# Optimization experiments

Measured on AMD Instinct MI355X. Metric: run time of the kernel, lower is better.

## Reference

```python
import jax, jax.numpy as jnp
import numpy as np
import math

B, L, DM, H, DK, DV, T, PW = 2, 512, 256, 4, 64, 64, 8, 8


def setup_inputs() -> dict:
    key = jax.random.key(0)
    ks = jax.random.split(key, 16)
    q = jax.random.normal(ks[0], (B, L, DM), jnp.float32)
    k = jax.random.normal(ks[1], (B, L, DM), jnp.float32)
    v = jax.random.normal(ks[2], (B, L, DM), jnp.float32)
    # sorted timestamps in [0, 100]
    t_in = jnp.sort(jax.random.uniform(ks[3], (B, L), jnp.float32) * 100.0, axis=-1)
    c = jax.random.randint(ks[4], (B, L), 0, T).astype(jnp.int32)  # no padding tokens
    mask = jnp.broadcast_to(jnp.triu(jnp.ones((L, L), bool), 1)[None], (B, L, L))  # causal
    s_in = 1.0 / math.sqrt(DM)
    Wq = jax.random.normal(ks[5], (DM, H * DK), jnp.float32) * s_in
    Wk = jax.random.normal(ks[6], (DM, H * DK), jnp.float32) * s_in
    Wv = jax.random.normal(ks[7], (DM, H * DV), jnp.float32) * s_in
    Wo = jax.random.normal(ks[8], (H * DV, DM), jnp.float32) / math.sqrt(H * DV)
    ln_g = jnp.ones((DM,), jnp.float32)
    ln_b = jnp.zeros((DM,), jnp.float32)
    # per-(type, head) phi MLP: Linear(1->PW), GELU, Linear(PW->PW), GELU, Linear(PW->1)
    W0 = jax.random.normal(ks[9], (T, H, PW, 1), jnp.float32) * 0.1
    b0 = jax.random.normal(ks[10], (T, H, PW), jnp.float32) * 0.1
    W1 = jax.random.normal(ks[11], (T, H, PW, PW), jnp.float32) * 0.3
    b1 = jax.random.normal(ks[12], (T, H, PW), jnp.float32) * 0.1
    Wf = jax.random.normal(ks[13], (T, H, 1, PW), jnp.float32) * 0.3
    bf = jax.random.normal(ks[14], (T, H, 1), jnp.float32) * 0.1
    return dict(q=q, k=k, v=v, t_in=t_in, c=c, mask=mask, ln_g=ln_g, ln_b=ln_b,
                Wq=Wq, Wk=Wk, Wv=Wv, Wo=Wo, W0=W0, b0=b0, W1=W1, b1=b1, Wf=Wf, bf=bf)


def _gelu(x):
    return jax.nn.gelu(x, approximate=False)


def _forward(q, k, v, t_in, c, mask, ln_g, ln_b, Wq, Wk, Wv, Wo, W0, b0, W1, b1, Wf, bf):
    Bb, Ll, dm = q.shape
    num_types, Hh, pw, _ = W0.shape
    dk = Wq.shape[1] // Hh
    dv = Wv.shape[1] // Hh
    scale = math.sqrt(dk)
    residual = q
    # pre-LayerNorm on q only (normalize_before=True)
    mu = jnp.mean(q, -1, keepdims=True)
    var = jnp.mean((q - mu) ** 2, -1, keepdims=True)
    qn = (q - mu) / jnp.sqrt(var + 1e-6) * ln_g + ln_b
    qh = (qn @ Wq).reshape(Bb, Ll, Hh, dk).transpose(0, 2, 1, 3)  # (B,H,L,dk)
    kh = (k @ Wk).reshape(Bb, Ll, Hh, dk).transpose(0, 2, 1, 3)
    vh = (v @ Wv).reshape(Bb, Ll, Hh, dv).transpose(0, 2, 1, 3)
    delta = t_in[:, :, None] - t_in[:, None, :]  # (B,Li,Lj)
    valid = c < num_types
    vmask = valid[:, :, None] & valid[:, None, :]  # (B,Li,Lj)
    cs = jnp.clip(c, 0, num_types - 1)
    # gather per-token phi params -> leading dims (B,L,H,...)
    W0g = W0[cs][..., 0]          # (B,L,H,pw)
    b0g = b0[cs]                  # (B,L,H,pw)
    W1g = W1[cs]                  # (B,L,H,pw,pw)  [out,in]
    b1g = b1[cs]                  # (B,L,H,pw)
    Wfg = Wf[cs][:, :, :, 0, :]   # (B,L,H,pw)
    bfg = bf[cs][..., 0]          # (B,L,H)
    # phiQ[b,h,i,j] = phi_{c_i,h}(delta_ij)
    hq = _gelu(delta[:, :, None, :, None] * W0g[:, :, :, None, :] + b0g[:, :, :, None, :])  # (B,Li,H,Lj,pw)
    hq = _gelu(jnp.einsum('bihjw,bihuw->bihju', hq, W1g) + b1g[:, :, :, None, :])
    phiQ = jnp.einsum('bihjw,bihw->bihj', hq, Wfg) + bfg[:, :, :, None]  # (B,Li,H,Lj)
    phiQ = jnp.where(vmask[:, :, None, :], phiQ, 0.0).transpose(0, 2, 1, 3)  # (B,H,Li,Lj)
    # phiK[b,h,i,j] = phi_{c_j,h}(delta_ij)
    hk = _gelu(delta[:, :, :, None, None] * W0g[:, None, :, :, :] + b0g[:, None, :, :, :])  # (B,Li,Lj,H,pw)
    hk = _gelu(jnp.einsum('bijhw,bjhuw->bijhu', hk, W1g) + b1g[:, None, :, :, :])
    phiK = jnp.einsum('bijhw,bjhw->bijh', hk, Wfg) + bfg[:, None, :, :]  # (B,Li,Lj,H)
    phiK = jnp.where(vmask[:, :, :, None], phiK, 0.0).transpose(0, 3, 1, 2)  # (B,H,Li,Lj)
    # scores[b,h,i,j] = (q_i . k_j) * phiQ * phiK / scale  (equivalent to q_mod*k_mod sum)
    scores = jnp.einsum('bhid,bhjd->bhij', qh, kh) * phiQ * phiK / scale
    scores = jnp.where(mask[:, None, :, :], -jnp.inf, scores)
    attn = jax.nn.softmax(scores, axis=-1)
    # out_heads[b,h,i,d] = sum_j attn * phiK * v_j  (equivalent to einsum with v_mod)
    out_heads = jnp.einsum('bhij,bhjd->bhid', attn * phiK, vh)
    out = out_heads.transpose(0, 2, 1, 3).reshape(Bb, Ll, Hh * dv) @ Wo
    return out + residual


def reference(q, k, v, t_in, c, mask, ln_g, ln_b, Wq, Wk, Wv, Wo, W0, b0, W1, b1, Wf, bf):
    return _forward(q, k, v, t_in, c, mask, ln_g, ln_b, Wq, Wk, Wv, Wo, W0, b0, W1, b1, Wf, bf)
```

## Files before the change

### kernel.cpp

```cpp
#include <hip/hip_runtime.h>
#include <math.h>

#define B_  2
#define L_  512
#define DM_ 256
#define H_  4
#define DK_ 64
#define DV_ 64
#define T_  8
#define PW_ 8
#define NTAB 4096

typedef unsigned int uint;

__device__ __forceinline__ unsigned short f2b(float x) {
    uint u = __float_as_uint(x);
    u += 0x7fffu + ((u >> 16) & 1u);
    return (unsigned short)(u >> 16);
}
__device__ __forceinline__ float bl(uint u)  { return __uint_as_float(u << 16); }
__device__ __forceinline__ float bh_(uint u) { return __uint_as_float(u & 0xffff0000u); }

__device__ __forceinline__ float gelu_fast(float x) {
    const float z  = x * 0.70710678118654752440f;
    const float az = fabsf(z);
    const float t  = __builtin_amdgcn_rcpf(fmaf(0.3275911f, az, 1.0f));
    float p = fmaf(t, 1.061405429f, -1.453152027f);
    p = fmaf(t, p, 1.421413741f);
    p = fmaf(t, p, -0.284496736f);
    p = fmaf(t, p, 0.254829592f);
    p *= t;
    const float e  = __expf(-az * az);
    float er = fmaf(-p, e, 1.0f);
    er = copysignf(er, z);
    return 0.5f * x * (1.0f + er);
}

__device__ __forceinline__ float phi_eval_u(
        const float w0r[8], const float b0r[8], const float4* __restrict__ W14,
        const float b1r[8], const float wfr[8], float bfv, float delta) {
    float h1[PW_];
#pragma unroll
    for (int w = 0; w < PW_; ++w)
        h1[w] = gelu_fast(fmaf(delta, w0r[w], b0r[w]));
    float out = bfv;
#pragma unroll
    for (int u = 0; u < PW_; ++u) {
        const float4 c0 = W14[u * 2];
        const float4 c1 = W14[u * 2 + 1];
        float a = b1r[u];
        a = fmaf(c0.x, h1[0], a); a = fmaf(c0.y, h1[1], a);
        a = fmaf(c0.z, h1[2], a); a = fmaf(c0.w, h1[3], a);
        a = fmaf(c1.x, h1[4], a); a = fmaf(c1.y, h1[5], a);
        a = fmaf(c1.z, h1[6], a); a = fmaf(c1.w, h1[7], a);
        out = fmaf(wfr[u], gelu_fast(a), out);
    }
    return out;
}

__device__ __forceinline__ float tab_lerp(const float* __restrict__ tab, float delta) {
    float x = delta * ((float)(NTAB - 1) / 100.0f);
    x = fminf(fmaxf(x, 0.0f), (float)(NTAB - 1) - 0.001f);
    const int i0 = (int)x;
    const float f = x - (float)i0;
    const float a = tab[i0];
    const float b = tab[i0 + 1];
    return fmaf(b - a, f, a);
}

__global__ __launch_bounds__(256) void prep_kernel(
        const float* __restrict__ q, const float* __restrict__ k,
        const float* __restrict__ v, const float* __restrict__ ln_g,
        const float* __restrict__ ln_b, const float* __restrict__ Wq,
        const float* __restrict__ Wk, const float* __restrict__ Wv,
        const float* __restrict__ W0, const float* __restrict__ b0,
        const float* __restrict__ W1, const float* __restrict__ b1,
        const float* __restrict__ Wf, const float* __restrict__ bfp,
        float* __restrict__ qh, uint* __restrict__ khT,
        uint* __restrict__ vh8, float* __restrict__ tabs) {
    __shared__ __align__(16) float smem[8 * DM_];
    const int tid = threadIdx.x, lane = tid & 63, wv = tid >> 6;
    const int bx = blockIdx.x;

    if (bx < 512) {
        const int th = bx >> 4;
        const int p = (bx & 15) * 256 + tid;
        if (tid < 64) smem[tid] = W1[th * 64 + tid];
        float w0r[8], b0r[8], b1r[8], wfr[8];
#pragma unroll
        for (int w = 0; w < 8; ++w) {
            w0r[w] = W0[th * 8 + w]; b0r[w] = b0[th * 8 + w];
            b1r[w] = b1[th * 8 + w]; wfr[w] = Wf[th * 8 + w];
        }
        const float bfv = bfp[th];
        __syncthreads();
        const float delta = (float)p * (100.0f / (float)(NTAB - 1));
        tabs[th * NTAB + p] = phi_eval_u(w0r, b0r,
                                         reinterpret_cast<const float4*>(smem),
                                         b1r, wfr, bfv, delta);
    } else if (bx < 1024) {
        const bool isQ = (bx < 768);
        const int bid = isQ ? (bx - 512) : (bx - 768);
        float (*xr)[DM_] = reinterpret_cast<float (*)[DM_]>(smem);
        const int row0 = bid * 4;
        const int b = row0 >> 9;
        const int lrow0 = row0 & (L_ - 1);
        const float* src = isQ ? q : k;
        const float* W   = isQ ? Wq : Wk;
        for (int x = tid; x < 4 * DM_; x += 256)
            xr[x >> 8][x & 255] = src[(size_t)row0 * DM_ + x];
        __syncthreads();
        if (isQ) {
            const int r = wv;
            float x0 = xr[r][lane], x1 = xr[r][lane + 64];
            float x2 = xr[r][lane + 128], x3 = xr[r][lane + 192];
            float s = x0 + x1 + x2 + x3;
#pragma unroll
            for (int off = 32; off; off >>= 1) s += __shfl_xor(s, off);
            const float mean = s * (1.0f / 256.0f);
            x0 -= mean; x1 -= mean; x2 -= mean; x3 -= mean;
            float s2 = x0 * x0 + x1 * x1 + x2 * x2 + x3 * x3;
#pragma unroll
            for (int off = 32; off; off >>= 1) s2 += __shfl_xor(s2, off);
            const float rstd = rsqrtf(s2 * (1.0f / 256.0f) + 1e-6f);
            xr[r][lane]       = x0 * rstd * ln_g[lane]       + ln_b[lane];
            xr[r][lane + 64]  = x1 * rstd * ln_g[lane + 64]  + ln_b[lane + 64];
            xr[r][lane + 128] = x2 * rstd * ln_g[lane + 128] + ln_b[lane + 128];
            xr[r][lane + 192] = x3 * rstd * ln_g[lane + 192] + ln_b[lane + 192];
            __syncthreads();
        }
        float acc[4] = {0, 0, 0, 0};
#pragma unroll 8
        for (int kk = 0; kk < DM_; ++kk) {
            const float w = W[(size_t)kk * DM_ + tid];
#pragma unroll
            for (int r = 0; r < 4; ++r) acc[r] = fmaf(xr[r][kk], w, acc[r]);
        }
        if (isQ) {
#pragma unroll
            for (int r = 0; r < 4; ++r)
                qh[(size_t)(row0 + r) * DM_ + tid] = acc[r];
        } else {
            __syncthreads();
            unsigned short* sbuf = reinterpret_cast<unsigned short*>(smem);
#pragma unroll
            for (int r = 0; r < 4; ++r)
                sbuf[tid * 4 + r] = f2b(acc[r]);
            __syncthreads();
            if (tid < 128) {
                const int jl = tid & 3;
                const int g = tid >> 2;
                const int h2 = g >> 3, d8 = g & 7;
                unsigned short e[8];
#pragma unroll
                for (int ee = 0; ee < 8; ++ee)
                    e[ee] = sbuf[(h2 * 64 + d8 * 8 + ee) * 4 + jl];
                uint4 o;
                o.x = (uint)e[0] | ((uint)e[1] << 16);
                o.y = (uint)e[2] | ((uint)e[3] << 16);
                o.z = (uint)e[4] | ((uint)e[5] << 16);
                o.w = (uint)e[6] | ((uint)e[7] << 16);
                reinterpret_cast<uint4*>(khT)[
                    ((size_t)(b * H_ + h2) * 8 + d8) * L_ + lrow0 + jl] = o;
            }
        }
    } else {
        const int bid = bx - 1024;
        float (*xr)[DM_] = reinterpret_cast<float (*)[DM_]>(smem);
        const int row0 = bid * 8;
        const int b = row0 >> 9;
        const int lrow0 = row0 & (L_ - 1);
        for (int x = tid; x < 8 * DM_; x += 256)
            xr[x >> 8][x & 255] = v[(size_t)row0 * DM_ + x];
        __syncthreads();
        float acc[8] = {0, 0, 0, 0, 0, 0, 0, 0};
#pragma unroll 4
        for (int kk = 0; kk < DM_; ++kk) {
            const float w = Wv[(size_t)kk * DM_ + tid];
#pragma unroll
            for (int r = 0; r < 8; ++r) acc[r] = fmaf(xr[r][kk], w, acc[r]);
        }
        const int h = tid >> 6, d = tid & 63;
        const int bh = b * H_ + h;
        uint4 w4;
        w4.x = (uint)f2b(acc[0]) | ((uint)f2b(acc[1]) << 16);
        w4.y = (uint)f2b(acc[2]) | ((uint)f2b(acc[3]) << 16);
        w4.z = (uint)f2b(acc[4]) | ((uint)f2b(acc[5]) << 16);
        w4.w = (uint)f2b(acc[6]) | ((uint)f2b(acc[7]) << 16);
        reinterpret_cast<uint4*>(vh8)[((size_t)bh * 64 + (lrow0 >> 3)) * 64 + d] = w4;
    }
}

__global__ __launch_bounds__(64) void attn_kernel(
        const float* __restrict__ qh, const uint* __restrict__ khT,
        const uint* __restrict__ vh8, const float* __restrict__ t_in,
        const int* __restrict__ c, const float* __restrict__ tabs,
        float* __restrict__ oh) {
    __shared__ __align__(16) float qs[64];
    __shared__ __align__(16) float sw[L_];

    const int lane = threadIdx.x;
    const int unit = blockIdx.x;
    const int bh = unit & 7;
    const int b = bh >> 2, h = bh & 3;
    const int i = (L_ - 1) - (unit >> 3);
    const int row = b * L_ + i;

    qs[lane] = qh[(size_t)row * DM_ + h * DK_ + lane];
    const float ti = t_in[row];
    const int ciw = c[row];
    const bool vi = (ciw < T_);
    const float* tabQ = tabs + (size_t)(min(max(ciw, 0), T_ - 1) * H_ + h) * NTAB;
    __syncthreads();

    const float4* qs4 = reinterpret_cast<const float4*>(qs);
    const uint4* kT8 = reinterpret_cast<const uint4*>(khT) + (size_t)bh * 8 * L_;
    const float* tbase = t_in + b * L_;
    const int* cbase = c + b * L_;
    const int tmax = i >> 6;

    float s[8], pk[8];
    float m = -INFINITY;
#pragma unroll
    for (int t = 0; t < 8; ++t) {
        s[t] = -INFINITY; pk[t] = 0.0f;
        if (t <= tmax) {
            const int j = t * 64 + lane;
            const bool act = (j <= i);
            const float tj = tbase[j];
            const int cjw = cbase[j];
            const float* tabK = tabs + (size_t)(min(max(cjw, 0), T_ - 1) * H_ + h) * NTAB;
            const float delta = ti - tj;
            const float pq = vi ? tab_lerp(tabQ, delta) : 0.0f;
            const float pkv = (cjw < T_) ? tab_lerp(tabK, delta) : 0.0f;
            float dot = 0.0f;
#pragma unroll
            for (int d8 = 0; d8 < 8; ++d8) {
                const uint4 ku = kT8[(size_t)d8 * L_ + j];
                const float4 qa = qs4[2 * d8];
                const float4 qb = qs4[2 * d8 + 1];
                dot = fmaf(qa.x, bl(ku.x), fmaf(qa.y, bh_(ku.x),
                      fmaf(qa.z, bl(ku.y), fmaf(qa.w, bh_(ku.y), dot))));
                dot = fmaf(qb.x, bl(ku.z), fmaf(qb.y, bh_(ku.z),
                      fmaf(qb.z, bl(ku.w), fmaf(qb.w, bh_(ku.w), dot))));
            }
            if (act) { s[t] = dot * pq * pkv * 0.125f; pk[t] = pkv; }
            m = fmaxf(m, s[t]);
        }
    }
#pragma unroll
    for (int off = 32; off; off >>= 1) m = fmaxf(m, __shfl_xor(m, off));

    float l = 0.0f;
#pragma unroll
    for (int t = 0; t < 8; ++t) {
        if (t <= tmax) {
            const float e = __expf(s[t] - m);
            l += e;
            sw[t * 64 + lane] = e * pk[t];
        }
    }
#pragma unroll
    for (int off = 32; off; off >>= 1) l += __shfl_xor(l, off);
    __syncthreads();

    const uint4* vb = reinterpret_cast<const uint4*>(vh8) + (size_t)bh * 64 * 64 + lane;
    const int j8max = i >> 3;
    float a0 = 0.0f, a1 = 0.0f, a2 = 0.0f, a3 = 0.0f;
    int j8 = 0;
    for (; j8 + 1 <= j8max; j8 += 2) {
        const uint4 u0 = vb[(size_t)j8 * 64];
        const uint4 u1 = vb[(size_t)(j8 + 1) * 64];
        const float4 w0 = *reinterpret_cast<const float4*>(&sw[j8 * 8]);
        const float4 w1 = *reinterpret_cast<const float4*>(&sw[j8 * 8 + 4]);
        const float4 w2 = *reinterpret_cast<const float4*>(&sw[j8 * 8 + 8]);
        const float4 w3 = *reinterpret_cast<const float4*>(&sw[j8 * 8 + 12]);
        a0 = fmaf(w0.x, bl(u0.x), fmaf(w0.y, bh_(u0.x),
             fmaf(w0.z, bl(u0.y), fmaf(w0.w, bh_(u0.y), a0))));
        a1 = fmaf(w1.x, bl(u0.z), fmaf(w1.y, bh_(u0.z),
             fmaf(w1.z, bl(u0.w), fmaf(w1.w, bh_(u0.w), a1))));
        a2 = fmaf(w2.x, bl(u1.x), fmaf(w2.y, bh_(u1.x),
             fmaf(w2.z, bl(u1.y), fmaf(w2.w, bh_(u1.y), a2))));
        a3 = fmaf(w3.x, bl(u1.z), fmaf(w3.y, bh_(u1.z),
             fmaf(w3.z, bl(u1.w), fmaf(w3.w, bh_(u1.w), a3))));
    }
    for (; j8 <= j8max; ++j8) {
        const uint4 u = vb[(size_t)j8 * 64];
        const float4 w0 = *reinterpret_cast<const float4*>(&sw[j8 * 8]);
        const float4 w1 = *reinterpret_cast<const float4*>(&sw[j8 * 8 + 4]);
        a0 = fmaf(w0.x, bl(u.x), fmaf(w0.y, bh_(u.x),
             fmaf(w0.z, bl(u.y), fmaf(w0.w, bh_(u.y), a0))));
        a1 = fmaf(w1.x, bl(u.z), fmaf(w1.y, bh_(u.z),
             fmaf(w1.z, bl(u.w), fmaf(w1.w, bh_(u.w), a1))));
    }
    const float acc = (a0 + a1) + (a2 + a3);
    oh[(size_t)row * DM_ + h * DV_ + lane] = vi ? acc / l : 0.0f;
}

__global__ __launch_bounds__(256) void out4_kernel(const float* __restrict__ oh,
                                                   const float* __restrict__ Wo,
                                                   const float* __restrict__ q,
                                                   float* __restrict__ out) {
    __shared__ __align__(16) float xr[4][DM_];
    const int tid = threadIdx.x;
    const int row0 = blockIdx.x * 4;
    for (int x = tid; x < 4 * DM_; x += 256)
        xr[x >> 8][x & 255] = oh[(size_t)row0 * DM_ + x];
    __syncthreads();
    float acc[4] = {0, 0, 0, 0};
#pragma unroll 8
    for (int kk = 0; kk < DM_; ++kk) {
        const float w = Wo[(size_t)kk * DM_ + tid];
#pragma unroll
        for (int r = 0; r < 4; ++r) acc[r] = fmaf(xr[r][kk], w, acc[r]);
    }
#pragma unroll
    for (int r = 0; r < 4; ++r)
        out[(size_t)(row0 + r) * DM_ + tid] = acc[r] + q[(size_t)(row0 + r) * DM_ + tid];
}

extern "C" void kernel_launch(void* const* d_in, const int* in_sizes, int n_in,
                              void* d_out, int out_size, void* d_ws, size_t ws_size,
                              hipStream_t stream) {
    const float* q    = (const float*)d_in[0];
    const float* k    = (const float*)d_in[1];
    const float* v    = (const float*)d_in[2];
    const float* t_in = (const float*)d_in[3];
    const int*   c    = (const int*)d_in[4];
    const float* ln_g = (const float*)d_in[6];
    const float* ln_b = (const float*)d_in[7];
    const float* Wq   = (const float*)d_in[8];
    const float* Wk   = (const float*)d_in[9];
    const float* Wv   = (const float*)d_in[10];
    const float* Wo   = (const float*)d_in[11];
    const float* W0   = (const float*)d_in[12];
    const float* b0   = (const float*)d_in[13];
    const float* W1   = (const float*)d_in[14];
    const float* b1   = (const float*)d_in[15];
    const float* Wf   = (const float*)d_in[16];
    const float* bf   = (const float*)d_in[17];
    float* outp = (float*)d_out;

    const size_t SZ = (size_t)B_ * L_ * DM_;
    float* ws = (float*)d_ws;
    float* qh   = ws;
    uint*  khT  = (uint*)(ws + SZ);
    uint*  vh8  = (uint*)(ws + SZ + 131072);
    float* oh   = ws + SZ + 262144;
    float* tabs = ws + 2 * SZ + 262144;

    prep_kernel<<<dim3(1152), dim3(256), 0, stream>>>(
        q, k, v, ln_g, ln_b, Wq, Wk, Wv,
        W0, b0, W1, b1, Wf, bf, qh, khT, vh8, tabs);
    attn_kernel<<<dim3(4096), dim3(64), 0, stream>>>(
        qh, khT, vh8, t_in, c, tabs, oh);
    out4_kernel<<<dim3(256), dim3(256), 0, stream>>>(oh, Wo, q, outp);
}
```

Baseline: 46.72 us.

## Precompute causal QK dot products in a tiled GEMM kernel before attention

Adds a dots_kernel that computes q·k for all lower-triangular 64x64 tiles per (batch, head) using shared-memory register tiling, writing an fp32 score matrix to workspace. The attention kernel then reads a precomputed dot per (i,j) instead of recomputing each row's dot products from bf16 K with per-row Q. This trades redundant K reloads and per-row FMA work for an extra kernel launch and a 2x4x512x512 fp32 round trip through global memory.

```diff
diff --git a/kernel.cpp b/kernel.cpp
--- a/kernel.cpp
+++ b/kernel.cpp
@@ -191,12 +191,63 @@
     }
 }
 
+__global__ __launch_bounds__(256) void dots_kernel(
+        const float* __restrict__ qh, const uint* __restrict__ khT,
+        float* __restrict__ dots) {
+    __shared__ __align__(16) float Qs[64 * 65];
+    __shared__ __align__(16) float Ks[64 * 65];
+    const int tid = threadIdx.x;
+    const int bh = blockIdx.x & 7;
+    const int b = bh >> 2, h = bh & 3;
+    int tix = blockIdx.x >> 3;
+    int tj = 0;
+    while (tix >= 8 - tj) { tix -= 8 - tj; ++tj; }
+    const int ti = tj + tix;
+
+    for (int x = tid; x < 4096; x += 256) {
+        const int r = x >> 6, d = x & 63;
+        Qs[r * 65 + d] = qh[(size_t)(b * L_ + ti * 64 + r) * DM_ + h * DK_ + d];
+    }
+    for (int x = tid; x < 512; x += 256) {
+        const int cc = x & 63, d8 = x >> 6;
+        const uint4 ku = reinterpret_cast<const uint4*>(khT)[
+            ((size_t)bh * 8 + d8) * L_ + tj * 64 + cc];
+        float* kd = &Ks[cc * 65 + d8 * 8];
+        kd[0] = bl(ku.x); kd[1] = bh_(ku.x);
+        kd[2] = bl(ku.y); kd[3] = bh_(ku.y);
+        kd[4] = bl(ku.z); kd[5] = bh_(ku.z);
+        kd[6] = bl(ku.w); kd[7] = bh_(ku.w);
+    }
+    __syncthreads();
+
+    const int rg = tid >> 4, cg = tid & 15;
+    const int r0 = rg * 4, c0 = cg * 4;
+    float acc[4][4] = {{0,0,0,0},{0,0,0,0},{0,0,0,0},{0,0,0,0}};
+    for (int d = 0; d < 64; ++d) {
+        float qv[4], kv[4];
+#pragma unroll
+        for (int e = 0; e < 4; ++e) qv[e] = Qs[(r0 + e) * 65 + d];
+#pragma unroll
+        for (int e = 0; e < 4; ++e) kv[e] = Ks[(c0 + e) * 65 + d];
+#pragma unroll
+        for (int rr = 0; rr < 4; ++rr)
+#pragma unroll
+            for (int cc2 = 0; cc2 < 4; ++cc2)
+                acc[rr][cc2] = fmaf(qv[rr], kv[cc2], acc[rr][cc2]);
+    }
+#pragma unroll
+    for (int rr = 0; rr < 4; ++rr) {
+        float4 o;
+        o.x = acc[rr][0]; o.y = acc[rr][1]; o.z = acc[rr][2]; o.w = acc[rr][3];
+        *reinterpret_cast<float4*>(
+            &dots[((size_t)bh * L_ + ti * 64 + r0 + rr) * L_ + tj * 64 + c0]) = o;
+    }
+}
+
 __global__ __launch_bounds__(64) void attn_kernel(
-        const float* __restrict__ qh, const uint* __restrict__ khT,
-        const uint* __restrict__ vh8, const float* __restrict__ t_in,
-        const int* __restrict__ c, const float* __restrict__ tabs,
-        float* __restrict__ oh) {
-    __shared__ __align__(16) float qs[64];
+        const float* __restrict__ dots, const uint* __restrict__ vh8,
+        const float* __restrict__ t_in, const int* __restrict__ c,
+        const float* __restrict__ tabs, float* __restrict__ oh) {
     __shared__ __align__(16) float sw[L_];
 
     const int lane = threadIdx.x;
@@ -206,15 +257,12 @@
     const int i = (L_ - 1) - (unit >> 3);
     const int row = b * L_ + i;
 
-    qs[lane] = qh[(size_t)row * DM_ + h * DK_ + lane];
     const float ti = t_in[row];
     const int ciw = c[row];
     const bool vi = (ciw < T_);
     const float* tabQ = tabs + (size_t)(min(max(ciw, 0), T_ - 1) * H_ + h) * NTAB;
-    __syncthreads();
-
-    const float4* qs4 = reinterpret_cast<const float4*>(qs);
-    const uint4* kT8 = reinterpret_cast<const uint4*>(khT) + (size_t)bh * 8 * L_;
+
+    const float* dotrow = dots + ((size_t)bh * L_ + i) * L_;
     const float* tbase = t_in + b * L_;
     const int* cbase = c + b * L_;
     const int tmax = i >> 6;
@@ -227,24 +275,14 @@
         if (t <= tmax) {
             const int j = t * 64 + lane;
             const bool act = (j <= i);
+            const float dv = dotrow[j];
             const float tj = tbase[j];
             const int cjw = cbase[j];
             const float* tabK = tabs + (size_t)(min(max(cjw, 0), T_ - 1) * H_ + h) * NTAB;
             const float delta = ti - tj;
             const float pq = vi ? tab_lerp(tabQ, delta) : 0.0f;
             const float pkv = (cjw < T_) ? tab_lerp(tabK, delta) : 0.0f;
-            float dot = 0.0f;
-#pragma unroll
-            for (int d8 = 0; d8 < 8; ++d8) {
-                const uint4 ku = kT8[(size_t)d8 * L_ + j];
-                const float4 qa = qs4[2 * d8];
-                const float4 qb = qs4[2 * d8 + 1];
-                dot = fmaf(qa.x, bl(ku.x), fmaf(qa.y, bh_(ku.x),
-                      fmaf(qa.z, bl(ku.y), fmaf(qa.w, bh_(ku.y), dot))));
-                dot = fmaf(qb.x, bl(ku.z), fmaf(qb.y, bh_(ku.z),
-                      fmaf(qb.z, bl(ku.w), fmaf(qb.w, bh_(ku.w), dot))));
-            }
-            if (act) { s[t] = dot * pq * pkv * 0.125f; pk[t] = pkv; }
+            if (act) { s[t] = dv * pq * pkv * 0.125f; pk[t] = pkv; }
             m = fmaxf(m, s[t]);
         }
     }
@@ -348,11 +386,13 @@
     uint*  vh8  = (uint*)(ws + SZ + 131072);
     float* oh   = ws + SZ + 262144;
     float* tabs = ws + 2 * SZ + 262144;
+    float* dots = ws + 2 * SZ + 262144 + 131072;
 
     prep_kernel<<<dim3(1152), dim3(256), 0, stream>>>(
         q, k, v, ln_g, ln_b, Wq, Wk, Wv,
         W0, b0, W1, b1, Wf, bf, qh, khT, vh8, tabs);
+    dots_kernel<<<dim3(288), dim3(256), 0, stream>>>(qh, khT, dots);
     attn_kernel<<<dim3(4096), dim3(64), 0, stream>>>(
-        qh, khT, vh8, t_in, c, tabs, oh);
+        dots, vh8, t_in, c, tabs, oh);
     out4_kernel<<<dim3(256), dim3(256), 0, stream>>>(oh, Wo, q, outp);
 }
```

New measurement: 51.12 us. 1.09x slower.
